# Kernel optimization log

Measured on AMD Instinct MI355X. Metric: run time of the kernel, lower is better.

The kernel has to match this reference:

```python
import jax, jax.numpy as jnp
import numpy as np

EPS = 1e-5
NUM_GRAPHS = 512


def _glorot(key, shape):
    lim = float(np.sqrt(6.0 / (shape[0] + shape[1])))
    return jax.random.uniform(key, shape, jnp.float32, -lim, lim)


def setup_inputs() -> dict:
    key = jax.random.key(0)
    ks = jax.random.split(key, 20)
    N, E, F0 = 50000, 800000, 64
    x = jax.random.normal(ks[0], (N, F0), jnp.float32)
    edge_index = jax.random.randint(ks[1], (2, E), 0, N, jnp.int64)
    batch = jnp.sort(jax.random.randint(ks[2], (N,), 0, NUM_GRAPHS, jnp.int64))
    dims = [(F0, 128), (128, 64), (64, 32)]
    p = {}
    for i, (di, do) in enumerate(dims, start=1):
        p[f"W{i}l"] = _glorot(ks[3 * i], (di, do))
        p[f"b{i}"] = jnp.zeros((do,), jnp.float32)
        p[f"W{i}r"] = _glorot(ks[3 * i + 1], (di, do))
        p[f"g{i}"] = jnp.ones((do,), jnp.float32)
        p[f"be{i}"] = jnp.zeros((do,), jnp.float32)
    p["Wf1"] = _glorot(ks[13], (32, 128)); p["bf1"] = jnp.zeros((128,), jnp.float32)
    p["Wf2"] = _glorot(ks[14], (128, 64)); p["bf2"] = jnp.zeros((64,), jnp.float32)
    p["Wf3"] = _glorot(ks[15], (64, 2)); p["bf3"] = jnp.zeros((2,), jnp.float32)
    return {"x": x, "edge_index": edge_index, "batch": batch, **p}


def _sage(x, src, dst, Wl, bl, Wr, n):
    # mean-aggregate neighbor features (gather from src, scatter-mean to dst)
    agg = jax.ops.segment_sum(x[src], dst, num_segments=n)
    cnt = jax.ops.segment_sum(jnp.ones((src.shape[0],), x.dtype), dst, num_segments=n)
    mean = agg / jnp.maximum(cnt, 1.0)[:, None]
    return mean @ Wl + bl + x @ Wr


def _bn(x, g, b):
    mu = jnp.mean(x, axis=0)
    var = jnp.mean((x - mu) ** 2, axis=0)  # biased var, torch training mode
    return (x - mu) * jax.lax.rsqrt(var + EPS) * g + b


def reference(x, edge_index, batch,
              W1l, b1, W1r, g1, be1,
              W2l, b2, W2r, g2, be2,
              W3l, b3, W3r, g3, be3,
              Wf1, bf1, Wf2, bf2, Wf3, bf3):
    n = x.shape[0]
    src, dst = edge_index[0], edge_index[1]
    h = _bn(jax.nn.relu(_sage(x, src, dst, W1l, b1, W1r, n)), g1, be1)
    h = _bn(jax.nn.relu(_sage(h, src, dst, W2l, b2, W2r, n)), g2, be2)
    h = _bn(jax.nn.relu(_sage(h, src, dst, W3l, b3, W3r, n)), g3, be3)
    pooled = jax.ops.segment_sum(h, batch, num_segments=NUM_GRAPHS)  # [G, 32]
    cr = jax.nn.relu(pooled @ Wf1 + bf1)  # dropout = identity (eval)
    cr = jax.nn.relu(cr @ Wf2 + bf2)
    cr = cr @ Wf3 + bf3
    return cr.reshape(-1, 2)
```

## Files before the change

### kernel.cpp

```cpp
#include <hip/hip_runtime.h>
#include <hip/hip_bf16.h>

#define EPSBN 1e-5f
#define NGRAPH 512
#define SCAN_NB 128

typedef __attribute__((ext_vector_type(8))) short bf16x8;
typedef __attribute__((ext_vector_type(4))) float f32x4;

__device__ inline short f2bf(float f) {
    unsigned u = __builtin_bit_cast(unsigned, f);
    u += 0x7fffu + ((u >> 16) & 1u);
    return (short)(u >> 16);
}
__device__ inline float bf2f(short s) {
    unsigned u = ((unsigned)(unsigned short)s) << 16;
    return __builtin_bit_cast(float, u);
}

__global__ void __launch_bounds__(256) k_hist(
    const int* __restrict__ dst, int* __restrict__ hist,
    const int* __restrict__ batch, float* __restrict__ gcnt, int E, int N)
{
    const int stride = gridDim.x * 256;
    for (int e = blockIdx.x * 256 + threadIdx.x; e < E; e += stride)
        atomicAdd(&hist[dst[e]], 1);
    for (int i = blockIdx.x * 256 + threadIdx.x; i < N; i += stride)
        atomicAdd(&gcnt[batch[i]], 1.0f);
}

__global__ void __launch_bounds__(256) k_scan1(
    const int* __restrict__ hist, int* __restrict__ blocksum, int N)
{
    __shared__ int red[256];
    const int C = (N + SCAN_NB - 1) / SCAN_NB;
    const int b = blockIdx.x, t = threadIdx.x;
    const int lo = b * C, hi = min(lo + C, N);
    int s = 0;
    for (int i = lo + t; i < hi; i += 256) s += hist[i];
    red[t] = s;
    __syncthreads();
    for (int off = 128; off; off >>= 1) {
        if (t < off) red[t] += red[t + off];
        __syncthreads();
    }
    if (t == 0) blocksum[b] = red[0];
}

__global__ void __launch_bounds__(256) k_scan3(
    const int* __restrict__ hist, const int* __restrict__ blocksum,
    int* __restrict__ row_off, int* __restrict__ cursor, int N)
{
    __shared__ int red[256];
    __shared__ int boff_s;
    const int C = (N + SCAN_NB - 1) / SCAN_NB;
    const int b = blockIdx.x, t = threadIdx.x;
    const int lo = b * C, hi = min(lo + C, N);
    if (t == 0) {
        int acc = 0;
        for (int i = 0; i < b; i++) acc += blocksum[i];
        boff_s = acc;
        if (b == SCAN_NB - 1) {
            int tot = acc;
            for (int i = b; i < SCAN_NB; i++) tot += blocksum[i];
            row_off[N] = tot;
        }
    }
    const int TC = (C + 255) / 256;
    const int s0 = lo + t * TC;
    const int s1 = min(s0 + TC, hi);
    int s = 0;
    for (int i = s0; i < s1; i++) s += hist[i];
    red[t] = s;
    __syncthreads();
    for (int off = 1; off < 256; off <<= 1) {
        int u = (t >= off) ? red[t - off] : 0;
        __syncthreads();
        red[t] += u;
        __syncthreads();
    }
    int run = boff_s + red[t] - s;
    for (int i = s0; i < s1; i++) {
        row_off[i] = run;
        cursor[i] = run;
        run += hist[i];
    }
}

__global__ void __launch_bounds__(256) k_scatter(
    const int* __restrict__ src, const int* __restrict__ dst,
    int* __restrict__ cursor, int* __restrict__ csr, int E)
{
    for (int e = blockIdx.x * 256 + threadIdx.x; e < E; e += gridDim.x * 256) {
        int d = dst[e];
        int p = atomicAdd(&cursor[d], 1);
        csr[p] = src[e];
    }
}

template <int F>
__global__ void __launch_bounds__(256) k_gatherb(
    const short* __restrict__ feat, const int* __restrict__ row_off,
    const int* __restrict__ csr, short* __restrict__ aggb, int N)
{
    constexpr int LPR = F / 8;
    constexpr int RPB = 256 / LPR;
    const int lane = threadIdx.x % LPR;
    const int rloc = threadIdx.x / LPR;
    const short* fbase = feat + lane * 8;
    for (int row = blockIdx.x * RPB + rloc; row < N; row += gridDim.x * RPB) {
        const int s0 = row_off[row];
        const int s1 = row_off[row + 1];
        float acc0[8], acc1[8], acc2[8], acc3[8];
        #pragma unroll
        for (int i = 0; i < 8; i++) {
            acc0[i] = 0.f; acc1[i] = 0.f; acc2[i] = 0.f; acc3[i] = 0.f;
        }
        int p = s0;
        for (; p + 3 < s1; p += 4) {
            int sA = csr[p], sB = csr[p + 1], sC = csr[p + 2], sD = csr[p + 3];
            bf16x8 va = *(const bf16x8*)&fbase[(long long)sA * F];
            bf16x8 vb = *(const bf16x8*)&fbase[(long long)sB * F];
            bf16x8 vc = *(const bf16x8*)&fbase[(long long)sC * F];
            bf16x8 vd = *(const bf16x8*)&fbase[(long long)sD * F];
            #pragma unroll
            for (int i = 0; i < 8; i++) {
                acc0[i] += bf2f(va[i]);
                acc1[i] += bf2f(vb[i]);
                acc2[i] += bf2f(vc[i]);
                acc3[i] += bf2f(vd[i]);
            }
        }
        for (; p < s1; p++) {
            int sA = csr[p];
            bf16x8 va = *(const bf16x8*)&fbase[(long long)sA * F];
            #pragma unroll
            for (int i = 0; i < 8; i++) acc0[i] += bf2f(va[i]);
        }
        short o[8];
        #pragma unroll
        for (int i = 0; i < 8; i++)
            o[i] = f2bf((acc0[i] + acc1[i]) + (acc2[i] + acc3[i]));
        *(bf16x8*)&aggb[(long long)row * F + lane * 8] = *(bf16x8*)o;
    }
}

__global__ void __launch_bounds__(256) k_cvt(
    const float* __restrict__ in, short* __restrict__ out, long long n4)
{
    long long i = (long long)blockIdx.x * 256 + threadIdx.x;
    if (i >= n4) return;
    float4 v = *(const float4*)&in[i * 4];
    short4 o = make_short4(f2bf(v.x), f2bf(v.y), f2bf(v.z), f2bf(v.w));
    *(short4*)&out[i * 4] = o;
}

template <int K, int F, bool AFF>
__global__ void __launch_bounds__(64) k_wprep2(
    const float* __restrict__ Wl, const float* __restrict__ Wr,
    const float* __restrict__ a, const float* __restrict__ c,
    const float* __restrict__ bias,
    short* __restrict__ Wlt, short* __restrict__ Wrt,
    float* __restrict__ cvl, float* __restrict__ cvr)
{
    int j = blockIdx.x * 64 + threadIdx.x;
    const bool second = j >= F;
    const int jj = second ? j - F : j;
    if (jj >= F || j >= 2 * F) return;
    const float* W = second ? Wr : Wl;
    short* Wt = second ? Wrt : Wlt;
    float cv = (second && bias) ? bias[jj] : 0.f;
    for (int k = 0; k < K; k++) {
        float w = W[k * F + jj];
        float aa = 1.f;
        if constexpr (AFF) {
            aa = a[k];
            cv += c[k] * w;
        }
        Wt[jj * K + k] = f2bf(aa * w);
    }
    if (second) cvr[jj] = cv; else cvl[jj] = cv;
}

template <int K, int FOUT, bool DUAL, bool HASBASE, bool FINAL, bool OUTBF16,
          bool POOL>
__global__ void __launch_bounds__(256) k_mgemm(
    const short* __restrict__ A, const short* __restrict__ A2,
    const short* __restrict__ Wt, const short* __restrict__ Wt2,
    const float* __restrict__ cvec, const short* __restrict__ base,
    const int* __restrict__ row_off, void* outv,
    float* __restrict__ s_out, float* __restrict__ q_out,
    const int* __restrict__ batchp, float* __restrict__ praw, int N)
{
    constexpr int KS = K / 32;
    constexpr int NCT = FOUT / 16;
    const int lane = threadIdx.x & 63;
    const int wid = threadIdx.x >> 6;
    const int g = lane >> 4;
    const int mi = lane & 15;
    const int RT = (N + 15) >> 4;
    const int nw = gridDim.x * 4;
    float* outf = (float*)outv;
    short* outb = (short*)outv;

    float st_s[FINAL ? NCT : 1];
    float st_q[FINAL ? NCT : 1];
    if constexpr (FINAL) {
        #pragma unroll
        for (int ct = 0; ct < NCT; ct++) { st_s[ct] = 0.f; st_q[ct] = 0.f; }
    }

    for (int rt = blockIdx.x * 4 + wid; rt < RT; rt += nw) {
        const int m0 = rt * 16;
        int arow = m0 + mi;
        if (arow >= N) arow = N - 1;

        bf16x8 af[KS];
        bf16x8 af2[DUAL ? KS : 1];
        const short* ap = A + (long long)arow * K;
        #pragma unroll
        for (int s = 0; s < KS; s++)
            af[s] = *(const bf16x8*)(ap + s * 32 + g * 8);
        if constexpr (DUAL) {
            const short* ap2 = A2 + (long long)arow * K;
            #pragma unroll
            for (int s = 0; s < KS; s++)
                af2[s] = *(const bf16x8*)(ap2 + s * 32 + g * 8);
        }

        float invc[4];
        if constexpr (DUAL || HASBASE) {
            #pragma unroll
            for (int r = 0; r < 4; r++) {
                int row = m0 + 4 * g + r;
                int cnt = 1;
                if (row < N) cnt = max(row_off[row + 1] - row_off[row], 1);
                invc[r] = 1.f / (float)cnt;
            }
        }
        int bidx[4];
        if constexpr (POOL) {
            #pragma unroll
            for (int r = 0; r < 4; r++) {
                int row = m0 + 4 * g + r;
                bidx[r] = (row < N) ? batchp[row] : -1;
            }
        }

        #pragma unroll
        for (int ct = 0; ct < NCT; ct++) {
            f32x4 acc = {0.f, 0.f, 0.f, 0.f};
            f32x4 acc2 = {0.f, 0.f, 0.f, 0.f};
            const short* bp = Wt + (long long)(ct * 16 + mi) * K;
            #pragma unroll
            for (int s = 0; s < KS; s++) {
                bf16x8 bf = *(const bf16x8*)(bp + s * 32 + g * 8);
                acc = __builtin_amdgcn_mfma_f32_16x16x32_bf16(af[s], bf, acc, 0, 0, 0);
                if constexpr (DUAL) {
                    bf16x8 bf2 = *(const bf16x8*)(Wt2 + (long long)(ct * 16 + mi) * K + s * 32 + g * 8);
                    acc2 = __builtin_amdgcn_mfma_f32_16x16x32_bf16(af2[s], bf2, acc2, 0, 0, 0);
                }
            }
            float cv = cvec[ct * 16 + mi];
            float sl = 0.f, ql = 0.f;
            #pragma unroll
            for (int r = 0; r < 4; r++) {
                int row = m0 + 4 * g + r;
                if (row < N) {
                    float v = acc[r] + cv;
                    if constexpr (DUAL) v = fmaf(invc[r], acc2[r], v);
                    if constexpr (HASBASE)
                        v = fmaf(invc[r], bf2f(base[(long long)row * FOUT + ct * 16 + mi]), v);
                    if constexpr (FINAL) v = fmaxf(v, 0.f);
                    if constexpr (POOL) {
                        atomicAdd(&praw[bidx[r] * FOUT + ct * 16 + mi], v);
                    } else if constexpr (OUTBF16) {
                        outb[(long long)row * FOUT + ct * 16 + mi] = f2bf(v);
                    } else {
                        outf[(long long)row * FOUT + ct * 16 + mi] = v;
                    }
                    if constexpr (FINAL) { sl += v; ql += v * v; }
                }
            }
            if constexpr (FINAL) {
                sl += __shfl_xor(sl, 16, 64);
                sl += __shfl_xor(sl, 32, 64);
                ql += __shfl_xor(ql, 16, 64);
                ql += __shfl_xor(ql, 32, 64);
                st_s[ct] += sl;
                st_q[ct] += ql;
            }
        }
    }

    if constexpr (FINAL) {
        __shared__ float redS[4][NCT][16];
        __shared__ float redQ[4][NCT][16];
        if (lane < 16) {
            #pragma unroll
            for (int ct = 0; ct < NCT; ct++) {
                redS[wid][ct][lane] = st_s[ct];
                redQ[wid][ct][lane] = st_q[ct];
            }
        }
        __syncthreads();
        if (wid == 0 && lane < 16) {
            #pragma unroll
            for (int ct = 0; ct < NCT; ct++) {
                float s = redS[0][ct][lane] + redS[1][ct][lane] +
                          redS[2][ct][lane] + redS[3][ct][lane];
                float q = redQ[0][ct][lane] + redQ[1][ct][lane] +
                          redQ[2][ct][lane] + redQ[3][ct][lane];
                atomicAdd(&s_out[ct * 16 + lane], s);
                atomicAdd(&q_out[ct * 16 + lane], q);
            }
        }
    }
}

__global__ void k_finalize(const float* __restrict__ s, const float* __restrict__ q,
                           const float* __restrict__ g, const float* __restrict__ be,
                           float* __restrict__ a, float* __restrict__ c,
                           int F, float invN)
{
    int j = threadIdx.x;
    if (j < F) {
        float mu = s[j] * invN;
        float var = q[j] * invN - mu * mu;
        float aj = g[j] / sqrtf(var + EPSBN);
        a[j] = aj;
        c[j] = be[j] - mu * aj;
    }
}

__global__ void __launch_bounds__(128) k_mlp(
    const float* __restrict__ praw, const float* __restrict__ a3,
    const float* __restrict__ c3, const float* __restrict__ gcnt,
    const float* __restrict__ Wf1, const float* __restrict__ bf1,
    const float* __restrict__ Wf2, const float* __restrict__ bf2,
    const float* __restrict__ Wf3, const float* __restrict__ bf3,
    float* __restrict__ out)
{
    __shared__ float p[32], h1[128], h2[64];
    int g = blockIdx.x, t = threadIdx.x;
    if (t < 32) p[t] = a3[t] * praw[g * 32 + t] + gcnt[g] * c3[t];
    __syncthreads();
    {
        float acc = bf1[t];
        #pragma unroll
        for (int k = 0; k < 32; k++) acc += p[k] * Wf1[k * 128 + t];
        h1[t] = fmaxf(acc, 0.f);
    }
    __syncthreads();
    if (t < 64) {
        float acc = bf2[t];
        #pragma unroll
        for (int k = 0; k < 128; k++) acc += h1[k] * Wf2[k * 64 + t];
        h2[t] = fmaxf(acc, 0.f);
    }
    __syncthreads();
    if (t < 2) {
        float acc = bf3[t];
        #pragma unroll
        for (int k = 0; k < 64; k++) acc += h2[k] * Wf3[k * 2 + t];
        out[g * 2 + t] = acc;
    }
}

extern "C" void kernel_launch(void* const* d_in, const int* in_sizes, int n_in,
                              void* d_out, int out_size, void* d_ws, size_t ws_size,
                              hipStream_t stream)
{
    const float* x     = (const float*)d_in[0];
    const int*   ei    = (const int*)d_in[1];
    const int*   batch = (const int*)d_in[2];
    const float* W1l = (const float*)d_in[3];
    const float* b1  = (const float*)d_in[4];
    const float* W1r = (const float*)d_in[5];
    const float* g1  = (const float*)d_in[6];
    const float* be1 = (const float*)d_in[7];
    const float* W2l = (const float*)d_in[8];
    const float* b2  = (const float*)d_in[9];
    const float* W2r = (const float*)d_in[10];
    const float* g2  = (const float*)d_in[11];
    const float* be2 = (const float*)d_in[12];
    const float* W3l = (const float*)d_in[13];
    const float* b3  = (const float*)d_in[14];
    const float* W3r = (const float*)d_in[15];
    const float* g3  = (const float*)d_in[16];
    const float* be3 = (const float*)d_in[17];
    const float* Wf1 = (const float*)d_in[18];
    const float* bf1 = (const float*)d_in[19];
    const float* Wf2 = (const float*)d_in[20];
    const float* bf2 = (const float*)d_in[21];
    const float* Wf3 = (const float*)d_in[22];
    const float* bf3 = (const float*)d_in[23];

    const int N = in_sizes[0] / 64;
    const int E = in_sizes[1] / 2;
    const int* src = ei;
    const int* dst = ei + E;

    char* ws = (char*)d_ws;
    size_t off = 0;
    auto alloc = [&](size_t bytes) {
        size_t o = off;
        off += (bytes + 511) & ~(size_t)511;
        return o;
    };
    const size_t o_rowoff = alloc((size_t)(N + 1) * 4);
    const size_t o_cursor = alloc((size_t)N * 4);
    const size_t o_bsum   = alloc(SCAN_NB * 4);
    const size_t o_csr    = alloc((size_t)E * 4);
    const size_t o_zoneB  = alloc((size_t)N * 128);
    const size_t o_zoneC  = alloc((size_t)N * 128);
    const size_t o_zoneD  = alloc((size_t)N * 256);
    const size_t o_zoneE  = alloc((size_t)N * 128);
    const size_t o_aff    = alloc(448 * 4);
    const size_t o_cvec   = alloc(512 * 4);
    const size_t o_wt     = alloc((8192 * 4 + 2048 * 2) * 2);
    const size_t o_zero0  = off;
    const size_t o_hist   = alloc((size_t)N * 4);
    const size_t o_stats  = alloc(448 * 4);
    const size_t o_praw   = alloc((size_t)NGRAPH * 32 * 4);
    const size_t o_gcnt   = alloc((size_t)NGRAPH * 4);
    const size_t zero_len = off - o_zero0;
    (void)ws_size;

    int* row_off = (int*)(ws + o_rowoff);
    int* hist    = (int*)(ws + o_hist);
    int* cursor  = (int*)(ws + o_cursor);
    int* bsum    = (int*)(ws + o_bsum);
    int* csr     = (int*)(ws + o_csr);
    short* xb   = (short*)(ws + o_zoneB);
    short* y2b  = (short*)(ws + o_zoneB);
    short* aggb = (short*)(ws + o_zoneC);
    short* t2b  = (short*)(ws + o_zoneC);
    short* t1b  = (short*)(ws + o_zoneD);
    short* y3b  = (short*)(ws + o_zoneD);
    short* m2b  = (short*)(ws + o_zoneE);
    short* m3b  = (short*)(ws + o_zoneE);
    float* praw = (float*)(ws + o_praw);
    float* gcnt = (float*)(ws + o_gcnt);
    float* s1 = (float*)(ws + o_stats);
    float* q1 = s1 + 128;
    float* s2 = q1 + 128;
    float* q2 = s2 + 64;
    float* s3 = q2 + 64;
    float* q3 = s3 + 32;
    float* a1 = (float*)(ws + o_aff);
    float* c1 = a1 + 128;
    float* a2 = c1 + 128;
    float* c2 = a2 + 64;
    float* a3 = c2 + 64;
    float* c3 = a3 + 32;
    float* cv1l = (float*)(ws + o_cvec);
    float* cv1r = cv1l + 128;
    float* cv2l = cv1r + 128;
    float* cv2r = cv2l + 64;
    float* cv3l = cv2r + 64;
    float* cv3r = cv3l + 32;
    short* W1l_t = (short*)(ws + o_wt);
    short* W1r_t = W1l_t + 8192;
    short* W2l_t = W1r_t + 8192;
    short* W2r_t = W2l_t + 8192;
    short* W3l_t = W2r_t + 8192;
    short* W3r_t = W3l_t + 2048;

    const float invN = 1.0f / (float)N;
    const int MG = 512;

    hipMemsetAsync(ws + o_zero0, 0, zero_len, stream);

    k_hist<<<2048, 256, 0, stream>>>(dst, hist, batch, gcnt, E, N);
    k_scan1<<<SCAN_NB, 256, 0, stream>>>(hist, bsum, N);
    k_scan3<<<SCAN_NB, 256, 0, stream>>>(hist, bsum, row_off, cursor, N);
    k_scatter<<<2048, 256, 0, stream>>>(src, dst, cursor, csr, E);

    k_cvt<<<(int)(((long long)N * 16 + 255) / 256), 256, 0, stream>>>(
        x, xb, (long long)N * 16);
    k_wprep2<64, 128, false><<<4, 64, 0, stream>>>(
        W1l, W1r, nullptr, nullptr, b1, W1l_t, W1r_t, cv1l, cv1r);

    k_gatherb<64><<<(N + 31) / 32, 256, 0, stream>>>(
        xb, row_off, csr, aggb, N);
    k_mgemm<64, 128, true, false, true, true, false><<<MG, 256, 0, stream>>>(
        xb, aggb, W1r_t, W1l_t, cv1r, nullptr, row_off, t1b, s1, q1,
        nullptr, nullptr, N);
    k_finalize<<<1, 128, 0, stream>>>(s1, q1, g1, be1, a1, c1, 128, invN);

    k_wprep2<128, 64, true><<<2, 64, 0, stream>>>(
        W2l, W2r, a1, c1, b2, W2l_t, W2r_t, cv2l, cv2r);
    k_mgemm<128, 64, false, false, false, true, false><<<MG, 256, 0, stream>>>(
        t1b, nullptr, W2l_t, nullptr, cv2l, nullptr, row_off, y2b,
        nullptr, nullptr, nullptr, nullptr, N);
    k_gatherb<64><<<(N + 31) / 32, 256, 0, stream>>>(
        y2b, row_off, csr, m2b, N);
    k_mgemm<128, 64, false, true, true, true, false><<<MG, 256, 0, stream>>>(
        t1b, nullptr, W2r_t, nullptr, cv2r, m2b, row_off, t2b, s2, q2,
        nullptr, nullptr, N);
    k_finalize<<<1, 64, 0, stream>>>(s2, q2, g2, be2, a2, c2, 64, invN);

    k_wprep2<64, 32, true><<<1, 64, 0, stream>>>(
        W3l, W3r, a2, c2, b3, W3l_t, W3r_t, cv3l, cv3r);
    k_mgemm<64, 32, false, false, false, true, false><<<MG, 256, 0, stream>>>(
        t2b, nullptr, W3l_t, nullptr, cv3l, nullptr, row_off, y3b,
        nullptr, nullptr, nullptr, nullptr, N);
    k_gatherb<32><<<(N + 63) / 64, 256, 0, stream>>>(
        y3b, row_off, csr, m3b, N);
    k_mgemm<64, 32, false, true, true, false, true><<<MG, 256, 0, stream>>>(
        t2b, nullptr, W3r_t, nullptr, cv3r, m3b, row_off, nullptr, s3, q3,
        batch, praw, N);
    k_finalize<<<1, 32, 0, stream>>>(s3, q3, g3, be3, a3, c3, 32, invN);

    k_mlp<<<NGRAPH, 128, 0, stream>>>(praw, a3, c3, gcnt,
                                      Wf1, bf1, Wf2, bf2, Wf3, bf3,
                                      (float*)d_out);
}
```

Measured before the change: 333.9 us.

## Privatize atomics per XCD for histogram, CSR scatter, and pooling

Replaces the single global degree histogram with eight per-XCD copies selected through the XCC_ID hardware register, and sums them inside the scan kernels. The CSR scatter becomes a work-stealing pass in which each XCD first handles edges whose destination falls in its own node range, so cursor atomics stay local to one XCD's L2. Graph-pool atomics likewise go to per-XCD partial buffers that the MLP kernel reduces. Per-graph node counts now come from a binary search over the sorted batch array instead of atomics. The cost is extra memory, more zeroing, and the scatter kernel reading every edge up to eight times.

```diff
diff --git a/kernel.cpp b/kernel.cpp
--- a/kernel.cpp
+++ b/kernel.cpp
@@ -17,27 +17,35 @@
     unsigned u = ((unsigned)(unsigned short)s) << 16;
     return __builtin_bit_cast(float, u);
 }
-
-__global__ void __launch_bounds__(256) k_hist(
-    const int* __restrict__ dst, int* __restrict__ hist,
-    const int* __restrict__ batch, float* __restrict__ gcnt, int E, int N)
-{
+__device__ inline int xcd_id() {
+    int x;
+    asm volatile("s_getreg_b32 %0, hwreg(HW_REG_XCC_ID, 0, 4)" : "=s"(x));
+    return x & 7;
+}
+
+__global__ void __launch_bounds__(256) k_hist8(
+    const int* __restrict__ dst, int* __restrict__ hist8, int E, int Npad)
+{
+    int* h = hist8 + xcd_id() * Npad;
     const int stride = gridDim.x * 256;
     for (int e = blockIdx.x * 256 + threadIdx.x; e < E; e += stride)
-        atomicAdd(&hist[dst[e]], 1);
-    for (int i = blockIdx.x * 256 + threadIdx.x; i < N; i += stride)
-        atomicAdd(&gcnt[batch[i]], 1.0f);
+        atomicAdd(&h[dst[e]], 1);
 }
 
 __global__ void __launch_bounds__(256) k_scan1(
-    const int* __restrict__ hist, int* __restrict__ blocksum, int N)
+    const int* __restrict__ hist8, int* __restrict__ blocksum, int N, int Npad)
 {
     __shared__ int red[256];
     const int C = (N + SCAN_NB - 1) / SCAN_NB;
     const int b = blockIdx.x, t = threadIdx.x;
     const int lo = b * C, hi = min(lo + C, N);
     int s = 0;
-    for (int i = lo + t; i < hi; i += 256) s += hist[i];
+    for (int i = lo + t; i < hi; i += 256) {
+        int v = 0;
+        #pragma unroll
+        for (int c = 0; c < 8; c++) v += hist8[c * Npad + i];
+        s += v;
+    }
     red[t] = s;
     __syncthreads();
     for (int off = 128; off; off >>= 1) {
@@ -48,8 +56,8 @@
 }
 
 __global__ void __launch_bounds__(256) k_scan3(
-    const int* __restrict__ hist, const int* __restrict__ blocksum,
-    int* __restrict__ row_off, int* __restrict__ cursor, int N)
+    const int* __restrict__ hist8, const int* __restrict__ blocksum,
+    int* __restrict__ row_off, int* __restrict__ cursor, int N, int Npad)
 {
     __shared__ int red[256];
     __shared__ int boff_s;
@@ -69,8 +77,14 @@
     const int TC = (C + 255) / 256;
     const int s0 = lo + t * TC;
     const int s1 = min(s0 + TC, hi);
+    auto hsum = [&](int i) {
+        int v = 0;
+        #pragma unroll
+        for (int c = 0; c < 8; c++) v += hist8[c * Npad + i];
+        return v;
+    };
     int s = 0;
-    for (int i = s0; i < s1; i++) s += hist[i];
+    for (int i = s0; i < s1; i++) s += hsum(i);
     red[t] = s;
     __syncthreads();
     for (int off = 1; off < 256; off <<= 1) {
@@ -83,19 +97,55 @@
     for (int i = s0; i < s1; i++) {
         row_off[i] = run;
         cursor[i] = run;
-        run += hist[i];
-    }
-}
-
-__global__ void __launch_bounds__(256) k_scatter(
+        run += hsum(i);
+    }
+}
+
+#define SC_CHUNK 1024
+__global__ void __launch_bounds__(256) k_scatter_x(
     const int* __restrict__ src, const int* __restrict__ dst,
-    int* __restrict__ cursor, int* __restrict__ csr, int E)
-{
-    for (int e = blockIdx.x * 256 + threadIdx.x; e < E; e += gridDim.x * 256) {
-        int d = dst[e];
-        int p = atomicAdd(&cursor[d], 1);
-        csr[p] = src[e];
-    }
+    int* __restrict__ cursor, int* __restrict__ csr,
+    int* __restrict__ work, int E, int N)
+{
+    const int myx = xcd_id();
+    const int chunk = (N + 7) / 8;
+    __shared__ int base_s;
+    for (int pp = 0; pp < 8; pp++) {
+        const int p = (myx + pp) & 7;
+        const int lo = p * chunk;
+        const int hi = min(lo + chunk, N);
+        for (;;) {
+            __syncthreads();
+            if (threadIdx.x == 0) base_s = atomicAdd(&work[p], SC_CHUNK);
+            __syncthreads();
+            const int base = base_s;
+            if (base >= E) break;
+            const int end = min(base + SC_CHUNK, E);
+            for (int e = base + threadIdx.x; e < end; e += 256) {
+                int d = dst[e];
+                if (d >= lo && d < hi) {
+                    int pos = atomicAdd(&cursor[d], 1);
+                    csr[pos] = src[e];
+                }
+            }
+        }
+    }
+}
+
+__device__ inline int lbound(const int* __restrict__ a, int n, int v) {
+    int lo = 0, hi = n;
+    while (lo < hi) {
+        int mid = (lo + hi) >> 1;
+        if (a[mid] < v) lo = mid + 1; else hi = mid;
+    }
+    return lo;
+}
+__global__ void __launch_bounds__(256) k_gcnt_bs(
+    const int* __restrict__ batch, float* __restrict__ gcnt, int N)
+{
+    int g = blockIdx.x * 256 + threadIdx.x;
+    if (g < NGRAPH)
+        gcnt[g] = (float)(lbound(batch, N, g + 1) - lbound(batch, N, g));
 }
 
 template <int F>
@@ -190,7 +240,7 @@
     const float* __restrict__ cvec, const short* __restrict__ base,
     const int* __restrict__ row_off, void* outv,
     float* __restrict__ s_out, float* __restrict__ q_out,
-    const int* __restrict__ batchp, float* __restrict__ praw, int N)
+    const int* __restrict__ batchp, float* __restrict__ praw8, int N)
 {
     constexpr int KS = K / 32;
     constexpr int NCT = FOUT / 16;
@@ -202,6 +252,8 @@
     const int nw = gridDim.x * 4;
     float* outf = (float*)outv;
     short* outb = (short*)outv;
+    float* pr = nullptr;
+    if constexpr (POOL) pr = praw8 + (size_t)xcd_id() * NGRAPH * 32;
 
     float st_s[FINAL ? NCT : 1];
     float st_q[FINAL ? NCT : 1];
@@ -273,7 +325,7 @@
                         v = fmaf(invc[r], bf2f(base[(long long)row * FOUT + ct * 16 + mi]), v);
                     if constexpr (FINAL) v = fmaxf(v, 0.f);
                     if constexpr (POOL) {
-                        atomicAdd(&praw[bidx[r] * FOUT + ct * 16 + mi], v);
+                        atomicAdd(&pr[bidx[r] * FOUT + ct * 16 + mi], v);
                     } else if constexpr (OUTBF16) {
                         outb[(long long)row * FOUT + ct * 16 + mi] = f2bf(v);
                     } else {
@@ -334,7 +386,7 @@
 }
 
 __global__ void __launch_bounds__(128) k_mlp(
-    const float* __restrict__ praw, const float* __restrict__ a3,
+    const float* __restrict__ praw8, const float* __restrict__ a3,
     const float* __restrict__ c3, const float* __restrict__ gcnt,
     const float* __restrict__ Wf1, const float* __restrict__ bf1,
     const float* __restrict__ Wf2, const float* __restrict__ bf2,
@@ -343,7 +395,13 @@
 {
     __shared__ float p[32], h1[128], h2[64];
     int g = blockIdx.x, t = threadIdx.x;
-    if (t < 32) p[t] = a3[t] * praw[g * 32 + t] + gcnt[g] * c3[t];
+    if (t < 32) {
+        float s = 0.f;
+        #pragma unroll
+        for (int c = 0; c < 8; c++)
+            s += praw8[(size_t)c * NGRAPH * 32 + g * 32 + t];
+        p[t] = a3[t] * s + gcnt[g] * c3[t];
+    }
     __syncthreads();
     {
         float acc = bf1[t];
@@ -398,6 +456,7 @@
 
     const int N = in_sizes[0] / 64;
     const int E = in_sizes[1] / 2;
+    const int Npad = (N + 255) & ~255;
     const int* src = ei;
     const int* dst = ei + E;
 
@@ -419,19 +478,21 @@
     const size_t o_aff    = alloc(448 * 4);
     const size_t o_cvec   = alloc(512 * 4);
     const size_t o_wt     = alloc((8192 * 4 + 2048 * 2) * 2);
+    const size_t o_gcnt   = alloc((size_t)NGRAPH * 4);
     const size_t o_zero0  = off;
-    const size_t o_hist   = alloc((size_t)N * 4);
+    const size_t o_hist8  = alloc((size_t)Npad * 8 * 4);
     const size_t o_stats  = alloc(448 * 4);
-    const size_t o_praw   = alloc((size_t)NGRAPH * 32 * 4);
-    const size_t o_gcnt   = alloc((size_t)NGRAPH * 4);
+    const size_t o_praw8  = alloc((size_t)NGRAPH * 32 * 4 * 8);
+    const size_t o_work   = alloc(8 * 4);
     const size_t zero_len = off - o_zero0;
     (void)ws_size;
 
     int* row_off = (int*)(ws + o_rowoff);
-    int* hist    = (int*)(ws + o_hist);
+    int* hist8   = (int*)(ws + o_hist8);
     int* cursor  = (int*)(ws + o_cursor);
     int* bsum    = (int*)(ws + o_bsum);
     int* csr     = (int*)(ws + o_csr);
+    int* work    = (int*)(ws + o_work);
     short* xb   = (short*)(ws + o_zoneB);
     short* y2b  = (short*)(ws + o_zoneB);
     short* aggb = (short*)(ws + o_zoneC);
@@ -440,8 +501,8 @@
     short* y3b  = (short*)(ws + o_zoneD);
     short* m2b  = (short*)(ws + o_zoneE);
     short* m3b  = (short*)(ws + o_zoneE);
-    float* praw = (float*)(ws + o_praw);
-    float* gcnt = (float*)(ws + o_gcnt);
+    float* praw8 = (float*)(ws + o_praw8);
+    float* gcnt  = (float*)(ws + o_gcnt);
     float* s1 = (float*)(ws + o_stats);
     float* q1 = s1 + 128;
     float* s2 = q1 + 128;
@@ -472,10 +533,11 @@
 
     hipMemsetAsync(ws + o_zero0, 0, zero_len, stream);
 
-    k_hist<<<2048, 256, 0, stream>>>(dst, hist, batch, gcnt, E, N);
-    k_scan1<<<SCAN_NB, 256, 0, stream>>>(hist, bsum, N);
-    k_scan3<<<SCAN_NB, 256, 0, stream>>>(hist, bsum, row_off, cursor, N);
-    k_scatter<<<2048, 256, 0, stream>>>(src, dst, cursor, csr, E);
+    k_hist8<<<2048, 256, 0, stream>>>(dst, hist8, E, Npad);
+    k_scan1<<<SCAN_NB, 256, 0, stream>>>(hist8, bsum, N, Npad);
+    k_scan3<<<SCAN_NB, 256, 0, stream>>>(hist8, bsum, row_off, cursor, N, Npad);
+    k_scatter_x<<<1024, 256, 0, stream>>>(src, dst, cursor, csr, work, E, N);
+    k_gcnt_bs<<<2, 256, 0, stream>>>(batch, gcnt, N);
 
     k_cvt<<<(int)(((long long)N * 16 + 255) / 256), 256, 0, stream>>>(
         x, xb, (long long)N * 16);
@@ -510,10 +572,10 @@
         y3b, row_off, csr, m3b, N);
     k_mgemm<64, 32, false, true, true, false, true><<<MG, 256, 0, stream>>>(
         t2b, nullptr, W3r_t, nullptr, cv3r, m3b, row_off, nullptr, s3, q3,
-        batch, praw, N);
+        batch, praw8, N);
     k_finalize<<<1, 32, 0, stream>>>(s3, q3, g3, be3, a3, c3, 32, invN);
 
-    k_mlp<<<NGRAPH, 128, 0, stream>>>(praw, a3, c3, gcnt,
+    k_mlp<<<NGRAPH, 128, 0, stream>>>(praw8, a3, c3, gcnt,
                                       Wf1, bf1, Wf2, bf2, Wf3, bf3,
                                       (float*)d_out);
 }
```

Result: slower. 422.0 us (+26.4%).
